# Kernel optimization log

Measured on AMD Instinct MI355X. Metric: run time of the kernel, lower is better.

The kernel has to match this reference:

```python
import jax, jax.numpy as jnp
import numpy as np

B, S, E = 4, 2048, 1024
H, D = 16, 64
SCALE = D ** -0.5


def setup_inputs() -> dict:
    key = jax.random.key(0)
    ks = jax.random.split(key, 6)
    x = jax.random.normal(ks[0], (B, S, E), dtype=jnp.float32)
    # per-head projection weights stacked along head axis: [H, E, D]
    Wq = jax.random.normal(ks[1], (H, E, D), dtype=jnp.float32) * 0.02
    Wk = jax.random.normal(ks[2], (H, E, D), dtype=jnp.float32) * 0.02
    Wv = jax.random.normal(ks[3], (H, E, D), dtype=jnp.float32) * 0.02
    # output projection: concat(H*D) -> E, with bias (nn.Linear default)
    Wo = jax.random.normal(ks[4], (H * D, E), dtype=jnp.float32) * 0.02
    bo = jax.random.normal(ks[5], (E,), dtype=jnp.float32) * 0.02
    return {"x": x, "Wq": Wq, "Wk": Wk, "Wv": Wv, "Wo": Wo, "bo": bo}


def reference(x, Wq, Wk, Wv, Wo, bo):
    # batched QKV projections for all heads at once
    q = jnp.einsum('bse,hed->bhsd', x, Wq)
    k = jnp.einsum('bse,hed->bhsd', x, Wk)
    v = jnp.einsum('bse,hed->bhsd', x, Wv)
    # full (non-causal) attention, scores [b,h,s,s]
    scores = jnp.einsum('bhsd,bhtd->bhst', q, k) * SCALE
    attn = jax.nn.softmax(scores, axis=-1)
    o = jnp.einsum('bhst,bhtd->bhsd', attn, v)
    # concat heads in head order along feature dim -> [b,s,H*D]
    o = o.transpose(0, 2, 1, 3).reshape(x.shape[0], x.shape[1], -1)
    return o @ Wo + bo
```

## Files before the change

### kernel.cpp

```cpp
#include <hip/hip_runtime.h>
#include <hip/hip_fp16.h>
#include <stdint.h>

#define BB 4
#define SS 2048
#define EE 1024
#define HH 16
#define DD 64

typedef _Float16 half8 __attribute__((ext_vector_type(8)));
typedef __fp16 fp16x2 __attribute__((ext_vector_type(2)));
typedef float f32x4 __attribute__((ext_vector_type(4)));
typedef uint32_t u32;

#define MFMA32(a, b, c) __builtin_amdgcn_mfma_f32_16x16x32_f16((a), (b), (c), 0, 0, 0)

#define GLD_LDS16(g, l)                                                        \
  __builtin_amdgcn_global_load_lds(                                            \
      (const __attribute__((address_space(1))) u32*)(const void*)(g),          \
      (__attribute__((address_space(3))) u32*)(void*)(l), 16, 0, 0)

static __device__ __forceinline__ u32 pkh(float a, float b) {
  union { fp16x2 h; u32 u; } z;
  z.h = __builtin_amdgcn_cvt_pkrtz(a, b);
  return z.u;
}

__global__ __launch_bounds__(256) void conv_x_k(const float* __restrict__ x,
                                                _Float16* __restrict__ xh) {
  size_t i = ((size_t)blockIdx.x * 256 + threadIdx.x) * 8;
  f32x4 a = *(const f32x4*)(x + i);
  f32x4 b = *(const f32x4*)(x + i + 4);
  half8 o;
  o[0] = (_Float16)a[0]; o[1] = (_Float16)a[1];
  o[2] = (_Float16)a[2]; o[3] = (_Float16)a[3];
  o[4] = (_Float16)b[0]; o[5] = (_Float16)b[1];
  o[6] = (_Float16)b[2]; o[7] = (_Float16)b[3];
  *(half8*)(xh + i) = o;
}

__global__ __launch_bounds__(256) void conv_w_k(const float* __restrict__ Wq,
                                                const float* __restrict__ Wk,
                                                const float* __restrict__ Wv,
                                                _Float16* __restrict__ Wt) {
  __shared__ float T[64][65];
  int bid = blockIdx.x;
  int sel = bid >> 8, rem = bid & 255;
  int h = rem >> 4, e0 = (rem & 15) * 64;
  const float* W = (sel == 0 ? Wq : sel == 1 ? Wk : Wv) + (size_t)h * EE * DD;
  float scale = (sel == 0) ? 0.18033688011112042f : 1.0f;
  int tid = threadIdx.x;
  {
    int e = tid >> 2, d0 = (tid & 3) * 16;
#pragma unroll
    for (int i = 0; i < 4; ++i) {
      f32x4 v = *(const f32x4*)(W + (size_t)(e0 + e) * DD + d0 + i * 4);
      T[e][d0 + i * 4 + 0] = v[0];
      T[e][d0 + i * 4 + 1] = v[1];
      T[e][d0 + i * 4 + 2] = v[2];
      T[e][d0 + i * 4 + 3] = v[3];
    }
  }
  __syncthreads();
  {
    int d = tid >> 2, c0 = (tid & 3) * 16;
    half8 o0, o1;
#pragma unroll
    for (int i = 0; i < 8; ++i) o0[i] = (_Float16)(T[c0 + i][d] * scale);
#pragma unroll
    for (int i = 0; i < 8; ++i) o1[i] = (_Float16)(T[c0 + 8 + i][d] * scale);
    _Float16* dst = Wt + ((size_t)sel * 1024 + h * 64 + d) * EE + e0 + c0;
    *(half8*)dst = o0;
    *(half8*)(dst + 8) = o1;
  }
}

__global__ __launch_bounds__(256) void conv_wo_k(const float* __restrict__ Wo,
                                                 _Float16* __restrict__ Wot) {
  __shared__ float T[64][65];
  int bid = blockIdx.x;
  int k0 = (bid >> 4) * 64, n0 = (bid & 15) * 64;
  int tid = threadIdx.x;
  {
    int k = tid >> 2, c0 = (tid & 3) * 16;
#pragma unroll
    for (int i = 0; i < 4; ++i) {
      f32x4 v = *(const f32x4*)(Wo + (size_t)(k0 + k) * EE + n0 + c0 + i * 4);
      T[k][c0 + i * 4 + 0] = v[0];
      T[k][c0 + i * 4 + 1] = v[1];
      T[k][c0 + i * 4 + 2] = v[2];
      T[k][c0 + i * 4 + 3] = v[3];
    }
  }
  __syncthreads();
  {
    int n = tid >> 2, c0 = (tid & 3) * 16;
    half8 o0, o1;
#pragma unroll
    for (int i = 0; i < 8; ++i) o0[i] = (_Float16)T[c0 + i][n];
#pragma unroll
    for (int i = 0; i < 8; ++i) o1[i] = (_Float16)T[c0 + 8 + i][n];
    _Float16* dst = Wot + (size_t)(n0 + n) * EE + k0 + c0;
    *(half8*)dst = o0;
    *(half8*)(dst + 8) = o1;
  }
}

__global__ __launch_bounds__(256, 3) void qkv_proj_k(
    const _Float16* __restrict__ xh, const _Float16* __restrict__ Wt,
    _Float16* __restrict__ qkv) {
  __shared__ __align__(16) _Float16 As[128 * 32];
  __shared__ __align__(16) _Float16 Bs[128 * 32];
  int bid = blockIdx.x;
  int nblk = bid % 24, mblk = bid / 24;
  int row0 = mblk * 128, n0 = nblk * 128;
  int tid = threadIdx.x, lane = tid & 63, w = tid >> 6;
  int wm = w >> 1, wn = w & 1;
  int l15 = lane & 15, lhi = lane >> 4;

  f32x4 acc[4][4];
#pragma unroll
  for (int i = 0; i < 4; ++i)
#pragma unroll
    for (int j = 0; j < 4; ++j) acc[i][j] = (f32x4){0.f, 0.f, 0.f, 0.f};

  const char* Ab = (const char*)xh + (size_t)row0 * 2048;
  const char* Bb = (const char*)Wt + (size_t)n0 * 2048;
  int ob0 = w * 1024 + lane * 16;

  for (int k0 = 0; k0 < EE; k0 += 32) {
    __syncthreads();
    GLD_LDS16(Ab + (size_t)(ob0 >> 6) * 2048 + k0 * 2 + (ob0 & 63),
              (char*)As + w * 1024);
    GLD_LDS16(Ab + (size_t)((ob0 + 4096) >> 6) * 2048 + k0 * 2 + (ob0 & 63),
              (char*)As + 4096 + w * 1024);
    GLD_LDS16(Bb + (size_t)(ob0 >> 6) * 2048 + k0 * 2 + (ob0 & 63),
              (char*)Bs + w * 1024);
    GLD_LDS16(Bb + (size_t)((ob0 + 4096) >> 6) * 2048 + k0 * 2 + (ob0 & 63),
              (char*)Bs + 4096 + w * 1024);
    __syncthreads();
    half8 a[4], b[4];
#pragma unroll
    for (int mf = 0; mf < 4; ++mf)
      a[mf] = *(const half8*)(As + (wm * 64 + mf * 16 + l15) * 32 + 8 * lhi);
#pragma unroll
    for (int nf = 0; nf < 4; ++nf)
      b[nf] = *(const half8*)(Bs + (wn * 64 + nf * 16 + l15) * 32 + 8 * lhi);
#pragma unroll
    for (int mf = 0; mf < 4; ++mf)
#pragma unroll
      for (int nf = 0; nf < 4; ++nf)
        acc[mf][nf] = MFMA32(a[mf], b[nf], acc[mf][nf]);
  }

  const size_t KOFF = (size_t)BB * HH * SS * DD;
#pragma unroll
  for (int mf = 0; mf < 4; ++mf)
#pragma unroll
    for (int nf = 0; nf < 4; ++nf)
#pragma unroll
      for (int r = 0; r < 4; ++r) {
        int row = row0 + wm * 64 + mf * 16 + 4 * lhi + r;
        int n = n0 + wn * 64 + nf * 16 + l15;
        int sel = n >> 10, hh = (n >> 6) & 15, d = n & 63;
        int b_ = row >> 11, s = row & 2047;
        qkv[(size_t)sel * KOFF + (((size_t)b_ * HH + hh) * SS + s) * DD + d] =
            (_Float16)acc[mf][nf][r];
      }
}

__global__ __launch_bounds__(256, 2) void attn_k(const _Float16* __restrict__ qkv,
                                                 _Float16* __restrict__ ob) {
  __shared__ __align__(16) _Float16 Ks[2][64][72];
  __shared__ __align__(16) _Float16 Vt[2][64][72];

  const int bid = blockIdx.x;
  const int bh = bid >> 4, qb = bid & 15;
  const int b_ = bh >> 4, h = bh & 15;
  const size_t KOFF = (size_t)BB * HH * SS * DD;
  const _Float16* qp = qkv + (size_t)bh * SS * DD;
  const _Float16* kp = qkv + KOFF + (size_t)bh * SS * DD;
  const _Float16* vp = qkv + 2 * KOFF + (size_t)bh * SS * DD;

  const int tid = threadIdx.x, lane = tid & 63, w = tid >> 6;
  const int l15 = lane & 15, lhi = lane >> 4;
  const int q0 = qb * 128;

  half8 qf[2][2];
#pragma unroll
  for (int ekf = 0; ekf < 2; ++ekf)
#pragma unroll
    for (int nq = 0; nq < 2; ++nq)
      qf[ekf][nq] = *(const half8*)(qp +
          (size_t)(q0 + w * 32 + nq * 16 + l15) * DD + ekf * 32 + 8 * lhi);

  f32x4 oacc[4][2];
#pragma unroll
  for (int i = 0; i < 4; ++i)
#pragma unroll
    for (int j = 0; j < 2; ++j) oacc[i][j] = (f32x4){0.f, 0.f, 0.f, 0.f};
  float rs[2] = {0.f, 0.f};

  const int trow = tid >> 3;
  const int c0h = (tid & 7) * 8;
  const int vsw = 16 * (tid & 7);

  {
    half8 kr0 = *(const half8*)(kp + (size_t)trow * DD + c0h);
    half8 kr1 = *(const half8*)(kp + (size_t)(trow + 32) * DD + c0h);
    half8 vr0 = *(const half8*)(vp + (size_t)trow * DD + c0h);
    half8 vr1 = *(const half8*)(vp + (size_t)(trow + 32) * DD + c0h);
    char* kd = (char*)&Ks[0][0][0];
    char* vd = (char*)&Vt[0][0][0];
    *(half8*)(kd + trow * 144 + c0h * 2) = kr0;
    *(half8*)(kd + (trow + 32) * 144 + c0h * 2) = kr1;
#pragma unroll
    for (int i = 0; i < 8; ++i) {
      *(_Float16*)(vd + (c0h + i) * 144 + ((2 * trow) ^ vsw)) = vr0[i];
      *(_Float16*)(vd + (c0h + i) * 144 + ((2 * (trow + 32)) ^ vsw)) = vr1[i];
    }
  }
  __syncthreads();

  const int srcA = l15 + 32 * (lhi & 1);
  const int srcB = srcA + 16;
  const bool sel_lo = (lhi < 2);
  const int NT = SS / 64;

  half8 kr0, kr1, vr0, vr1;
  for (int it = 0; it < NT; ++it) {
    const int cur = it & 1;
    if (it < NT - 1) {
      const _Float16* kt = kp + (size_t)(it + 1) * 64 * DD;
      const _Float16* vt = vp + (size_t)(it + 1) * 64 * DD;
      kr0 = *(const half8*)(kt + (size_t)trow * DD + c0h);
      kr1 = *(const half8*)(kt + (size_t)(trow + 32) * DD + c0h);
      vr0 = *(const half8*)(vt + (size_t)trow * DD + c0h);
      vr1 = *(const half8*)(vt + (size_t)(trow + 32) * DD + c0h);
    }
    const char* kb = (const char*)&Ks[cur][0][0];
    const char* vb = (const char*)&Vt[cur][0][0];

    f32x4 sac[4][2];
#pragma unroll
    for (int i = 0; i < 4; ++i)
#pragma unroll
      for (int j = 0; j < 2; ++j) sac[i][j] = (f32x4){0.f, 0.f, 0.f, 0.f};
#pragma unroll
    for (int ekf = 0; ekf < 2; ++ekf) {
      half8 kA[4];
#pragma unroll
      for (int nt = 0; nt < 4; ++nt)
        kA[nt] = *(const half8*)(kb + (size_t)((nt * 16 + l15) * 144 +
                                               ekf * 64 + 16 * lhi));
#pragma unroll
      for (int nt = 0; nt < 4; ++nt)
#pragma unroll
        for (int nq = 0; nq < 2; ++nq)
          sac[nt][nq] = MFMA32(kA[nt], qf[ekf][nq], sac[nt][nq]);
    }

    u32 pw[4][2][2];
#pragma unroll
    for (int nt = 0; nt < 4; ++nt)
#pragma unroll
      for (int nq = 0; nq < 2; ++nq) {
        float e0 = __builtin_amdgcn_exp2f(sac[nt][nq][0]);
        float e1 = __builtin_amdgcn_exp2f(sac[nt][nq][1]);
        float e2 = __builtin_amdgcn_exp2f(sac[nt][nq][2]);
        float e3 = __builtin_amdgcn_exp2f(sac[nt][nq][3]);
        rs[nq] += (e0 + e1) + (e2 + e3);
        pw[nt][nq][0] = pkh(e0, e1);
        pw[nt][nq][1] = pkh(e2, e3);
      }

#pragma unroll
    for (int kf = 0; kf < 2; ++kf) {
      half8 vA[4];
#pragma unroll
      for (int md = 0; md < 4; ++md) {
        int swz = 16 * ((2 * md + (l15 >> 3)) & 7);
        vA[md] = *(const half8*)(vb + (size_t)((md * 16 + l15) * 144 +
                                               ((64 * kf + 16 * lhi) ^ swz)));
      }
#pragma unroll
      for (int nq = 0; nq < 2; ++nq) {
        u32 w0a = (u32)__shfl((int)pw[2 * kf][nq][0], srcA, 64);
        u32 w0b = (u32)__shfl((int)pw[2 * kf + 1][nq][0], srcA, 64);
        u32 w1a = (u32)__shfl((int)pw[2 * kf][nq][1], srcA, 64);
        u32 w1b = (u32)__shfl((int)pw[2 * kf + 1][nq][1], srcA, 64);
        u32 w2a = (u32)__shfl((int)pw[2 * kf][nq][0], srcB, 64);
        u32 w2b = (u32)__shfl((int)pw[2 * kf + 1][nq][0], srcB, 64);
        u32 w3a = (u32)__shfl((int)pw[2 * kf][nq][1], srcB, 64);
        u32 w3b = (u32)__shfl((int)pw[2 * kf + 1][nq][1], srcB, 64);
        union { u32 u[4]; half8 h; } pb;
        pb.u[0] = sel_lo ? w0a : w0b;
        pb.u[1] = sel_lo ? w1a : w1b;
        pb.u[2] = sel_lo ? w2a : w2b;
        pb.u[3] = sel_lo ? w3a : w3b;
#pragma unroll
        for (int md = 0; md < 4; ++md)
          oacc[md][nq] = MFMA32(vA[md], pb.h, oacc[md][nq]);
      }
    }

    if (it < NT - 1) {
      char* kd = (char*)&Ks[cur ^ 1][0][0];
      char* vd = (char*)&Vt[cur ^ 1][0][0];
      *(half8*)(kd + trow * 144 + c0h * 2) = kr0;
      *(half8*)(kd + (trow + 32) * 144 + c0h * 2) = kr1;
#pragma unroll
      for (int i = 0; i < 8; ++i) {
        *(_Float16*)(vd + (c0h + i) * 144 + ((2 * trow) ^ vsw)) = vr0[i];
        *(_Float16*)(vd + (c0h + i) * 144 + ((2 * (trow + 32)) ^ vsw)) = vr1[i];
      }
    }
    __syncthreads();
  }

  float inv[2];
#pragma unroll
  for (int nq = 0; nq < 2; ++nq) {
    float t = rs[nq];
    t += __shfl_xor(t, 16, 64);
    t += __shfl_xor(t, 32, 64);
    inv[nq] = 1.0f / t;
  }
#pragma unroll
  for (int md = 0; md < 4; ++md)
#pragma unroll
    for (int nq = 0; nq < 2; ++nq)
#pragma unroll
      for (int r = 0; r < 4; ++r) {
        int q = q0 + w * 32 + nq * 16 + l15;
        int d = md * 16 + 4 * lhi + r;
        ob[((size_t)b_ * SS + q) * (HH * DD) + h * DD + d] =
            (_Float16)(oacc[md][nq][r] * inv[nq]);
      }
}

__global__ __launch_bounds__(256, 3) void oproj_k(
    const _Float16* __restrict__ ob, const _Float16* __restrict__ Wot,
    const float* __restrict__ bo, float* __restrict__ out) {
  __shared__ __align__(16) _Float16 As[128 * 32];
  __shared__ __align__(16) _Float16 Bs[128 * 32];
  int bid = blockIdx.x;
  int nblk = bid & 7, mblk = bid >> 3;
  int row0 = mblk * 128, n0 = nblk * 128;
  int tid = threadIdx.x, lane = tid & 63, w = tid >> 6;
  int wm = w >> 1, wn = w & 1;
  int l15 = lane & 15, lhi = lane >> 4;

  f32x4 acc[4][4];
#pragma unroll
  for (int i = 0; i < 4; ++i)
#pragma unroll
    for (int j = 0; j < 4; ++j) acc[i][j] = (f32x4){0.f, 0.f, 0.f, 0.f};

  const char* Ab = (const char*)ob + (size_t)row0 * 2048;
  const char* Bb = (const char*)Wot + (size_t)n0 * 2048;
  int ob0 = w * 1024 + lane * 16;

  for (int k0 = 0; k0 < EE; k0 += 32) {
    __syncthreads();
    GLD_LDS16(Ab + (size_t)(ob0 >> 6) * 2048 + k0 * 2 + (ob0 & 63),
              (char*)As + w * 1024);
    GLD_LDS16(Ab + (size_t)((ob0 + 4096) >> 6) * 2048 + k0 * 2 + (ob0 & 63),
              (char*)As + 4096 + w * 1024);
    GLD_LDS16(Bb + (size_t)(ob0 >> 6) * 2048 + k0 * 2 + (ob0 & 63),
              (char*)Bs + w * 1024);
    GLD_LDS16(Bb + (size_t)((ob0 + 4096) >> 6) * 2048 + k0 * 2 + (ob0 & 63),
              (char*)Bs + 4096 + w * 1024);
    __syncthreads();
    half8 a[4], b[4];
#pragma unroll
    for (int mf = 0; mf < 4; ++mf)
      a[mf] = *(const half8*)(As + (wm * 64 + mf * 16 + l15) * 32 + 8 * lhi);
#pragma unroll
    for (int nf = 0; nf < 4; ++nf)
      b[nf] = *(const half8*)(Bs + (wn * 64 + nf * 16 + l15) * 32 + 8 * lhi);
#pragma unroll
    for (int mf = 0; mf < 4; ++mf)
#pragma unroll
      for (int nf = 0; nf < 4; ++nf)
        acc[mf][nf] = MFMA32(a[mf], b[nf], acc[mf][nf]);
  }

#pragma unroll
  for (int mf = 0; mf < 4; ++mf)
#pragma unroll
    for (int nf = 0; nf < 4; ++nf) {
      int n = n0 + wn * 64 + nf * 16 + l15;
      float bias = bo[n];
#pragma unroll
      for (int r = 0; r < 4; ++r) {
        int row = row0 + wm * 64 + mf * 16 + 4 * lhi + r;
        out[(size_t)row * EE + n] = acc[mf][nf][r] + bias;
      }
    }
}

extern "C" void kernel_launch(void* const* d_in, const int* in_sizes, int n_in,
                              void* d_out, int out_size, void* d_ws, size_t ws_size,
                              hipStream_t stream) {
  const float* x  = (const float*)d_in[0];
  const float* Wq = (const float*)d_in[1];
  const float* Wk = (const float*)d_in[2];
  const float* Wv = (const float*)d_in[3];
  const float* Wo = (const float*)d_in[4];
  const float* bo = (const float*)d_in[5];
  float* out = (float*)d_out;

  _Float16* qkv = (_Float16*)d_ws;
  _Float16* obuf = qkv + (size_t)3 * BB * HH * SS * DD;
  _Float16* xh = (_Float16*)d_out;
  _Float16* Wt = xh + (size_t)BB * SS * EE;
  _Float16* Wot = qkv;

  conv_x_k<<<dim3(4096), dim3(256), 0, stream>>>(x, xh);
  conv_w_k<<<dim3(768), dim3(256), 0, stream>>>(Wq, Wk, Wv, Wt);
  qkv_proj_k<<<dim3(64 * 24), dim3(256), 0, stream>>>(xh, Wt, qkv);
  attn_k<<<dim3(64 * 16), dim3(256), 0, stream>>>(qkv, obuf);
  conv_wo_k<<<dim3(256), dim3(256), 0, stream>>>(Wo, Wot);
  oproj_k<<<dim3(64 * 8), dim3(256), 0, stream>>>(obuf, Wot, bo, out);
}
```

Baseline: 227.6 us.

## Pre-transpose V and stream K/V tiles into LDS via direct global-to-LDS loads

```diff
diff --git a/kernel.cpp b/kernel.cpp
--- a/kernel.cpp
+++ b/kernel.cpp
@@ -106,6 +106,33 @@
   }
 }
 
+__global__ __launch_bounds__(256) void vtrans_k(const _Float16* __restrict__ v,
+                                                _Float16* __restrict__ vT) {
+  __shared__ _Float16 T[64][72];
+  int bid = blockIdx.x;
+  int bh = bid >> 5, st = bid & 31;
+  const _Float16* vp = v + (size_t)bh * SS * DD + (size_t)st * 64 * DD;
+  _Float16* op = vT + (size_t)bh * DD * SS + (size_t)st * 64;
+  int tid = threadIdx.x;
+  {
+    int r = tid >> 2, c0 = (tid & 3) * 16;
+    half8 a = *(const half8*)(vp + (size_t)r * DD + c0);
+    half8 b = *(const half8*)(vp + (size_t)r * DD + c0 + 8);
+#pragma unroll
+    for (int j = 0; j < 8; ++j) T[c0 + j][r] = a[j];
+#pragma unroll
+    for (int j = 0; j < 8; ++j) T[c0 + 8 + j][r] = b[j];
+  }
+  __syncthreads();
+  {
+    int d = tid >> 2, sc = (tid & 3) * 16;
+    half8 o0 = *(const half8*)&T[d][sc];
+    half8 o1 = *(const half8*)&T[d][sc + 8];
+    *(half8*)(op + (size_t)d * SS + sc) = o0;
+    *(half8*)(op + (size_t)d * SS + sc + 8) = o1;
+  }
+}
+
 __global__ __launch_bounds__(256, 3) void qkv_proj_k(
     const _Float16* __restrict__ xh, const _Float16* __restrict__ Wt,
     _Float16* __restrict__ qkv) {
@@ -169,18 +196,19 @@
       }
 }
 
-__global__ __launch_bounds__(256, 2) void attn_k(const _Float16* __restrict__ qkv,
-                                                 _Float16* __restrict__ ob) {
-  __shared__ __align__(16) _Float16 Ks[2][64][72];
-  __shared__ __align__(16) _Float16 Vt[2][64][72];
+__global__ __launch_bounds__(256, 4) void attn_k(
+    const _Float16* __restrict__ qkv, const _Float16* __restrict__ vT,
+    _Float16* __restrict__ ob) {
+  __shared__ __align__(16) _Float16 Ks[64 * 64];
+  __shared__ __align__(16) _Float16 Vs[64 * 64];
 
   const int bid = blockIdx.x;
   const int bh = bid >> 4, qb = bid & 15;
   const int b_ = bh >> 4, h = bh & 15;
   const size_t KOFF = (size_t)BB * HH * SS * DD;
   const _Float16* qp = qkv + (size_t)bh * SS * DD;
-  const _Float16* kp = qkv + KOFF + (size_t)bh * SS * DD;
-  const _Float16* vp = qkv + 2 * KOFF + (size_t)bh * SS * DD;
+  const char* kp = (const char*)(qkv + KOFF + (size_t)bh * SS * DD);
+  const char* vtp = (const char*)(vT + (size_t)bh * DD * SS);
 
   const int tid = threadIdx.x, lane = tid & 63, w = tid >> 6;
   const int l15 = lane & 15, lhi = lane >> 4;
@@ -201,45 +229,25 @@
     for (int j = 0; j < 2; ++j) oacc[i][j] = (f32x4){0.f, 0.f, 0.f, 0.f};
   float rs[2] = {0.f, 0.f};
 
-  const int trow = tid >> 3;
-  const int c0h = (tid & 7) * 8;
-  const int vsw = 16 * (tid & 7);
-
-  {
-    half8 kr0 = *(const half8*)(kp + (size_t)trow * DD + c0h);
-    half8 kr1 = *(const half8*)(kp + (size_t)(trow + 32) * DD + c0h);
-    half8 vr0 = *(const half8*)(vp + (size_t)trow * DD + c0h);
-    half8 vr1 = *(const half8*)(vp + (size_t)(trow + 32) * DD + c0h);
-    char* kd = (char*)&Ks[0][0][0];
-    char* vd = (char*)&Vt[0][0][0];
-    *(half8*)(kd + trow * 144 + c0h * 2) = kr0;
-    *(half8*)(kd + (trow + 32) * 144 + c0h * 2) = kr1;
-#pragma unroll
-    for (int i = 0; i < 8; ++i) {
-      *(_Float16*)(vd + (c0h + i) * 144 + ((2 * trow) ^ vsw)) = vr0[i];
-      *(_Float16*)(vd + (c0h + i) * 144 + ((2 * (trow + 32)) ^ vsw)) = vr1[i];
-    }
-  }
-  __syncthreads();
+  const int prow = tid >> 3;
+  const int swz = ((tid & 7) * 16) ^ (16 * (prow & 7));
+  const int lds0 = tid * 16;
+  const int kg0 = prow * 128 + swz;
+  const int vg0 = prow * 4096 + swz;
+  const int xsw = 16 * (l15 & 7);
 
   const int srcA = l15 + 32 * (lhi & 1);
   const int srcB = srcA + 16;
   const bool sel_lo = (lhi < 2);
   const int NT = SS / 64;
 
-  half8 kr0, kr1, vr0, vr1;
   for (int it = 0; it < NT; ++it) {
-    const int cur = it & 1;
-    if (it < NT - 1) {
-      const _Float16* kt = kp + (size_t)(it + 1) * 64 * DD;
-      const _Float16* vt = vp + (size_t)(it + 1) * 64 * DD;
-      kr0 = *(const half8*)(kt + (size_t)trow * DD + c0h);
-      kr1 = *(const half8*)(kt + (size_t)(trow + 32) * DD + c0h);
-      vr0 = *(const half8*)(vt + (size_t)trow * DD + c0h);
-      vr1 = *(const half8*)(vt + (size_t)(trow + 32) * DD + c0h);
-    }
-    const char* kb = (const char*)&Ks[cur][0][0];
-    const char* vb = (const char*)&Vt[cur][0][0];
+    __syncthreads();
+    GLD_LDS16(kp + it * 8192 + kg0, (char*)Ks + lds0);
+    GLD_LDS16(kp + it * 8192 + 4096 + kg0, (char*)Ks + lds0 + 4096);
+    GLD_LDS16(vtp + it * 128 + vg0, (char*)Vs + lds0);
+    GLD_LDS16(vtp + it * 128 + 131072 + vg0, (char*)Vs + lds0 + 4096);
+    __syncthreads();
 
     f32x4 sac[4][2];
 #pragma unroll
@@ -251,8 +259,8 @@
       half8 kA[4];
 #pragma unroll
       for (int nt = 0; nt < 4; ++nt)
-        kA[nt] = *(const half8*)(kb + (size_t)((nt * 16 + l15) * 144 +
-                                               ekf * 64 + 16 * lhi));
+        kA[nt] = *(const half8*)((const char*)Ks + (nt * 16 + l15) * 128 +
+                                 ((64 * ekf + 16 * lhi) ^ xsw));
 #pragma unroll
       for (int nt = 0; nt < 4; ++nt)
 #pragma unroll
@@ -278,11 +286,9 @@
     for (int kf = 0; kf < 2; ++kf) {
       half8 vA[4];
 #pragma unroll
-      for (int md = 0; md < 4; ++md) {
-        int swz = 16 * ((2 * md + (l15 >> 3)) & 7);
-        vA[md] = *(const half8*)(vb + (size_t)((md * 16 + l15) * 144 +
-                                               ((64 * kf + 16 * lhi) ^ swz)));
-      }
+      for (int md = 0; md < 4; ++md)
+        vA[md] = *(const half8*)((const char*)Vs + (md * 16 + l15) * 128 +
+                                 ((64 * kf + 16 * lhi) ^ xsw));
 #pragma unroll
       for (int nq = 0; nq < 2; ++nq) {
         u32 w0a = (u32)__shfl((int)pw[2 * kf][nq][0], srcA, 64);
@@ -303,19 +309,6 @@
           oacc[md][nq] = MFMA32(vA[md], pb.h, oacc[md][nq]);
       }
     }
-
-    if (it < NT - 1) {
-      char* kd = (char*)&Ks[cur ^ 1][0][0];
-      char* vd = (char*)&Vt[cur ^ 1][0][0];
-      *(half8*)(kd + trow * 144 + c0h * 2) = kr0;
-      *(half8*)(kd + (trow + 32) * 144 + c0h * 2) = kr1;
-#pragma unroll
-      for (int i = 0; i < 8; ++i) {
-        *(_Float16*)(vd + (c0h + i) * 144 + ((2 * trow) ^ vsw)) = vr0[i];
-        *(_Float16*)(vd + (c0h + i) * 144 + ((2 * (trow + 32)) ^ vsw)) = vr1[i];
-      }
-    }
-    __syncthreads();
   }
 
   float inv[2];
@@ -411,16 +404,19 @@
   const float* bo = (const float*)d_in[5];
   float* out = (float*)d_out;
 
+  const size_t KOFF = (size_t)BB * HH * SS * DD;
   _Float16* qkv = (_Float16*)d_ws;
-  _Float16* obuf = qkv + (size_t)3 * BB * HH * SS * DD;
+  _Float16* obuf = qkv + 3 * KOFF;
   _Float16* xh = (_Float16*)d_out;
   _Float16* Wt = xh + (size_t)BB * SS * EE;
+  _Float16* vTbuf = xh;
   _Float16* Wot = qkv;
 
   conv_x_k<<<dim3(4096), dim3(256), 0, stream>>>(x, xh);
   conv_w_k<<<dim3(768), dim3(256), 0, stream>>>(Wq, Wk, Wv, Wt);
   qkv_proj_k<<<dim3(64 * 24), dim3(256), 0, stream>>>(xh, Wt, qkv);
-  attn_k<<<dim3(64 * 16), dim3(256), 0, stream>>>(qkv, obuf);
+  vtrans_k<<<dim3(64 * 32), dim3(256), 0, stream>>>(qkv + 2 * KOFF, vTbuf);
+  attn_k<<<dim3(64 * 16), dim3(256), 0, stream>>>(qkv, vTbuf, obuf);
   conv_wo_k<<<dim3(256), dim3(256), 0, stream>>>(Wo, Wot);
   oproj_k<<<dim3(64 * 8), dim3(256), 0, stream>>>(obuf, Wot, bo, out);
 }
```

Result: faster. 219.6 us (-3.5%).
